# Optimization experiments

Measured on AMD Instinct MI355X. Metric: run time of the kernel, lower is better.

Reference implementation:

```python
import jax, jax.numpy as jnp
import numpy as np

S, B, H, NH, M = 2048, 2, 2048, 16, 2048
D = H // NH
FF = 4 * H
NORM = float(np.sqrt(D))  # norm_factor = sqrt(head_dim), no layer scaling
MASK_FILL = jnp.float32(-1e4)


def _ln(x, g, b):
    mu = jnp.mean(x, -1, keepdims=True)
    var = jnp.mean(jnp.square(x - mu), -1, keepdims=True)
    return (x - mu) * jax.lax.rsqrt(var + 1e-5) * g + b


def _l2(x):  # F.normalize over last dim
    return x * jax.lax.rsqrt(jnp.sum(jnp.square(x), -1, keepdims=True) + 1e-12)


def _mlp(h, w1, b1, w2, b2):  # ParallelMLP: h -> 4h -> h with gelu
    return jax.nn.gelu(h @ w1 + b1) @ w2 + b2


def setup_inputs() -> dict:
    key = jax.random.key(0)
    ks = jax.random.split(key, 12)
    w = lambda k, sh: jax.random.normal(k, sh, jnp.float32) * 0.02
    return {
        'x': jax.random.normal(ks[0], (S, B, H), jnp.float32),
        'mem_hidden': jax.random.normal(ks[1], (M, B, H), jnp.float32),
        'mem_mask': jax.random.randint(ks[2], (B, 1, S, M), 0, 5) == 0,  # True = masked
        'ln1_g': jnp.ones((H,), jnp.float32), 'ln1_b': jnp.zeros((H,), jnp.float32),
        'ln2_g': jnp.ones((H,), jnp.float32), 'ln2_b': jnp.zeros((H,), jnp.float32),
        'ln3_g': jnp.ones((H,), jnp.float32), 'ln3_b': jnp.zeros((H,), jnp.float32),
        'w_mlp1_in': w(ks[3], (H, FF)), 'b_mlp1_in': jnp.zeros((FF,), jnp.float32),
        'w_mlp1_out': w(ks[4], (FF, H)), 'b_mlp1_out': jnp.zeros((H,), jnp.float32),
        'w_q': w(ks[5], (H, H)), 'b_q': jnp.zeros((H,), jnp.float32),
        'w_kv': w(ks[6], (H, 2 * H)), 'b_kv': jnp.zeros((2 * H,), jnp.float32),
        'w_dense': w(ks[7], (H, H)), 'b_dense': jnp.zeros((H,), jnp.float32),
        'w_mlp2_in': w(ks[8], (H, FF)), 'b_mlp2_in': jnp.zeros((FF,), jnp.float32),
        'w_mlp2_out': w(ks[9], (FF, H)), 'b_mlp2_out': jnp.zeros((H,), jnp.float32),
    }


def reference(x, mem_hidden, mem_mask, ln1_g, ln1_b, ln2_g, ln2_b, ln3_g, ln3_b,
              w_mlp1_in, b_mlp1_in, w_mlp1_out, b_mlp1_out,
              w_q, b_q, w_kv, b_kv, w_dense, b_dense,
              w_mlp2_in, b_mlp2_in, w_mlp2_out, b_mlp2_out):
    # NOTE: source literally replaces x with mlp1 output (no residual on mlp1)
    x = _mlp(_ln(x, ln1_g, ln1_b), w_mlp1_in, b_mlp1_in, w_mlp1_out, b_mlp1_out)

    # memory attention: l2-normalized query vs l2-normalized retrieved memory k/v
    h2 = _ln(x, ln2_g, ln2_b)
    q = _l2((h2 @ w_q + b_q).reshape(S, B, NH, D))              # [s,b,h,d]
    kv = (mem_hidden @ w_kv + b_kv).reshape(M, B, NH, 2 * D)    # hidden_to_kv
    k = _l2(kv[..., :D])                                        # [m,b,h,d]
    v = _l2(kv[..., D:])
    scores = jnp.einsum('sbhd,mbhd->bhsm', q, k) / NORM
    scores = jnp.where(mem_mask, MASK_FILL, scores)             # attention_mask_func fill
    probs = jax.nn.softmax(scores, axis=-1)
    ctx = jnp.einsum('bhsm,mbhd->sbhd', probs, v).reshape(S, B, H)
    x = x + ctx @ w_dense + b_dense                             # dense w/ skip_bias_add

    x = x + _mlp(_ln(x, ln3_g, ln3_b), w_mlp2_in, b_mlp2_in, w_mlp2_out, b_mlp2_out)
    return x
```

## Files before the change

kernel.cpp:

```cpp
#include <hip/hip_runtime.h>
#include <stdint.h>
#include <stddef.h>

typedef __attribute__((ext_vector_type(8))) short bf16x8;
typedef __attribute__((ext_vector_type(4))) float f32x4;
typedef __attribute__((ext_vector_type(16))) float f32x16;
typedef unsigned short u16;
typedef unsigned int u32;
typedef unsigned long long u64;

static constexpr int S_ = 2048, B_ = 2, H_ = 2048, NH_ = 16, D_ = 128, M_ = 2048, FF_ = 8192;
static constexpr int SB_ = S_ * B_;
static constexpr int MB_ = M_ * B_;

__device__ __forceinline__ float b2f(u16 b) {
  union { u32 u; float f; } v; v.u = ((u32)b) << 16; return v.f;
}
__device__ __forceinline__ u16 f2b(float f) {
  union { float f; u32 u; } v; v.f = f;
  u32 u = v.u;
  return (u16)((u + 0x7FFFu + ((u >> 16) & 1u)) >> 16);
}
__device__ __forceinline__ float geluf(float x) {
  float x3 = x * x * x;
  return 0.5f * x * (1.0f + tanhf(0.7978845608028654f * (x + 0.044715f * x3)));
}

#define LDSP(p) (reinterpret_cast<__attribute__((address_space(3))) uint32_t*>(reinterpret_cast<uintptr_t>(p)))
#define GLBP(p) (reinterpret_cast<const __attribute__((address_space(1))) uint32_t*>(reinterpret_cast<uintptr_t>(p)))

__global__ void detect_kinds(const u32* __restrict__ x0, const u32* __restrict__ mask, int* __restrict__ flags) {
  if (threadIdx.x == 0 && blockIdx.x == 0) {
    int cnt = 0;
    for (int i = 0; i < 256; ++i) {
      u32 e = (x0[i] >> 7) & 0xFFu;
      if (e >= 118u && e <= 130u) ++cnt;
    }
    flags[0] = (cnt >= 128) ? 0 : 1;
    int all01 = 1, allf = 1, allb = 1;
    for (int i = 0; i < 256; ++i) {
      u32 v = mask[i];
      if (v > 1u) all01 = 0;
      if (v != 0u && v != 0x3F800000u) allf = 0;
      u32 lo = v & 0xFFFFu, hi = v >> 16;
      if ((lo != 0u && lo != 0x3F80u) || (hi != 0u && hi != 0x3F80u)) allb = 0;
    }
    flags[1] = all01 ? 1 : (allf ? 3 : (allb ? 2 : 0));
  }
}

__global__ void mask_bits(const void* __restrict__ mraw, const int* __restrict__ flags, u64* __restrict__ bm) {
  int i = blockIdx.x * 256 + threadIdx.x;
  int kind = flags[1];
  int masked;
  if (kind == 1)      masked = ((const int*)mraw)[i] != 0;
  else if (kind == 3) masked = ((const float*)mraw)[i] != 0.0f;
  else if (kind == 2) masked = ((const u16*)mraw)[i] != 0;
  else                masked = ((const unsigned char*)mraw)[i] != 0;
  u64 vote = __ballot(masked == 0);
  if ((threadIdx.x & 63) == 0) bm[i >> 6] = vote;
}

__global__ void cvt_all(const void* s0, const void* s1, const void* s2, const void* s3,
                        const void* s4, const void* s5, const void* s6, const void* s7,
                        const void* s8, const void* s9, const void* s10, const void* s11,
                        const void* s12, const int* __restrict__ flags, float* __restrict__ SM) {
  const int i = blockIdx.x * 256 + threadIdx.x;
  if (i >= 40960) return;
  const void* src; int off;
  if (i < 8192)       { src = s0;  off = 0; }
  else if (i < 10240) { src = s1;  off = 8192; }
  else if (i < 12288) { src = s2;  off = 10240; }
  else if (i < 16384) { src = s3;  off = 12288; }
  else if (i < 18432) { src = s4;  off = 16384; }
  else if (i < 26624) { src = s5;  off = 18432; }
  else if (i < 28672) { src = s6;  off = 26624; }
  else if (i < 30720) { src = s7;  off = 28672; }
  else if (i < 32768) { src = s8;  off = 30720; }
  else if (i < 34816) { src = s9;  off = 32768; }
  else if (i < 36864) { src = s10; off = 34816; }
  else if (i < 38912) { src = s11; off = 36864; }
  else                { src = s12; off = 38912; }
  const int j = i - off;
  SM[i] = flags[0] ? ((const float*)src)[j] : b2f(((const u16*)src)[j]);
}

__global__ void cast_in_bf16(const void* __restrict__ src, const int* __restrict__ flags, u16* __restrict__ dst, int n8) {
  int i = blockIdx.x * 256 + threadIdx.x;
  if (i >= n8) return;
  if (flags[0]) {
    const float4* p = (const float4*)src;
    float4 a = p[i * 2], c = p[i * 2 + 1];
    bf16x8 o;
    o[0] = (short)f2b(a.x); o[1] = (short)f2b(a.y); o[2] = (short)f2b(a.z); o[3] = (short)f2b(a.w);
    o[4] = (short)f2b(c.x); o[5] = (short)f2b(c.y); o[6] = (short)f2b(c.z); o[7] = (short)f2b(c.w);
    *(bf16x8*)&dst[i * 8] = o;
  } else {
    *(bf16x8*)&dst[i * 8] = ((const bf16x8*)src)[i];
  }
}

__global__ __launch_bounds__(256) void transpose_cast(const void* __restrict__ in, const int* __restrict__ flags,
                                                      u16* __restrict__ out, int R, int C) {
  __shared__ u16 tile[64][65];
  const int isf = flags[0];
  const int tr = blockIdx.y * 64, tc = blockIdx.x * 64;
  const int tx = threadIdx.x & 63, ty = threadIdx.x >> 6;
  const float* inf = (const float*)in;
  const u16* inb = (const u16*)in;
#pragma unroll
  for (int i = 0; i < 16; ++i) {
    int r = ty * 16 + i;
    size_t idx = (size_t)(tr + r) * C + tc + tx;
    tile[r][tx] = isf ? f2b(inf[idx]) : inb[idx];
  }
  __syncthreads();
#pragma unroll
  for (int i = 0; i < 16; ++i) {
    int c = ty * 16 + i;
    out[(size_t)(tc + c) * R + tr + tx] = tile[tx][c];
  }
}

template <int EXT>
__global__ __launch_bounds__(256) void layernorm_k(const void* __restrict__ xin, const int* __restrict__ flags,
                                                   const float* __restrict__ g, const float* __restrict__ bta,
                                                   u16* __restrict__ out) {
  const int row = blockIdx.x, t = threadIdx.x;
  float v[8];
  bool bfmode = EXT && (flags[0] == 0);
  if (bfmode) {
    const u16* xr = (const u16*)xin + (size_t)row * H_ + t * 8;
    bf16x8 a = *(const bf16x8*)xr;
#pragma unroll
    for (int j = 0; j < 8; ++j) v[j] = b2f((u16)a[j]);
  } else {
    const float* xr = (const float*)xin + (size_t)row * H_ + t * 8;
    float4 a = *(const float4*)xr, c = *(const float4*)(xr + 4);
    v[0] = a.x; v[1] = a.y; v[2] = a.z; v[3] = a.w;
    v[4] = c.x; v[5] = c.y; v[6] = c.z; v[7] = c.w;
  }
  float s1 = 0.f, s2 = 0.f;
#pragma unroll
  for (int j = 0; j < 8; ++j) { s1 += v[j]; s2 += v[j] * v[j]; }
#pragma unroll
  for (int off = 32; off > 0; off >>= 1) { s1 += __shfl_down(s1, off); s2 += __shfl_down(s2, off); }
  __shared__ float red[8];
  const int w = t >> 6;
  if ((t & 63) == 0) { red[w] = s1; red[4 + w] = s2; }
  __syncthreads();
  s1 = red[0] + red[1] + red[2] + red[3];
  s2 = red[4] + red[5] + red[6] + red[7];
  const float mean = s1 * (1.0f / H_);
  const float rstd = rsqrtf(s2 * (1.0f / H_) - mean * mean + 1e-5f);
  bf16x8 o;
#pragma unroll
  for (int j = 0; j < 8; ++j) {
    float y = (v[j] - mean) * rstd * g[t * 8 + j] + bta[t * 8 + j];
    o[j] = (short)f2b(y);
  }
  *(bf16x8*)(out + (size_t)row * H_ + t * 8) = o;
}

template <int GELU, int RES, int WF, int WB, int ODYN>
__global__ __launch_bounds__(256, 2) void gemmra(const u16* __restrict__ A, const u16* __restrict__ Bt,
                                                 const float* __restrict__ bias, const float* __restrict__ res,
                                                 void* __restrict__ outF, u16* __restrict__ outB,
                                                 const int* __restrict__ flags, int Mr, int N, int K) {
  __shared__ u16 lds[32768];
  const int t = threadIdx.x;
  const int w = t >> 6, l = t & 63, lr = l & 15, lk = l >> 4;
  const int wr = w >> 1, wc = w & 1;
  const int gx = gridDim.x, gy = gridDim.y;
  const int orig = blockIdx.y * gx + blockIdx.x;
  const int nwg = gx * gy, per = nwg >> 3;
  int tm, tn;
  if ((gx & 7) == 0 && (per & 7) == 0) {
    const int xcd = orig & 7, p = orig >> 3;
    const int ncx = gx >> 3, cy = per >> 3;
    const int ccol = xcd % ncx, crow = xcd / ncx;
    const int px = p & 7, py = p >> 3;
    tn = (ccol * 8 + px) * 128;
    tm = (crow * cy + py) * 128;
  } else {
    tn = (orig % gx) * 128;
    tm = (orig / gx) * 128;
  }
  u32 aofs[4], bofs[4];
#pragma unroll
  for (int i = 0; i < 4; ++i) {
    const int idx = i * 256 + t;
    const int srow = idx >> 3, sc = idx & 7;
    const int lc = sc ^ (srow & 7);
    aofs[i] = (u32)(tm + srow) * (u32)K + (u32)lc * 8;
    bofs[i] = (u32)(tn + srow) * (u32)K + (u32)lc * 8;
  }
  const int wdst = w * 512;
  const int cso0 = ((0 + lk) ^ (lr & 7)) * 8;
  const int cso1 = ((4 + lk) ^ (lr & 7)) * 8;
  int arow[4], brow[4];
#pragma unroll
  for (int f = 0; f < 4; ++f) {
    arow[f] = (wr * 64 + f * 16 + lr) * 64;
    brow[f] = (wc * 64 + f * 16 + lr) * 64;
  }

  const int NS = K >> 6;
  f32x4 acc[4][4] = {};

#define STG(sl) do {                                                                                  \
    u16* Ad = lds + ((sl) & 1) * 16384;                                                               \
    u16* Bd = Ad + 8192;                                                                              \
    const u32 ko = (u32)(sl) * 64;                                                                    \
    _Pragma("unroll")                                                                                 \
    for (int i = 0; i < 4; ++i) {                                                                     \
      __builtin_amdgcn_global_load_lds(GLBP(A + aofs[i] + ko), LDSP(Ad + i * 2048 + wdst), 16, 0, 0); \
      __builtin_amdgcn_global_load_lds(GLBP(Bt + bofs[i] + ko), LDSP(Bd + i * 2048 + wdst), 16, 0, 0);\
    }                                                                                                 \
  } while (0)
#define RD(afX, bqX, sl, cso) do {                                                                    \
    const u16* As_ = lds + ((sl) & 1) * 16384;                                                        \
    const u16* Bs_ = As_ + 8192;                                                                      \
    _Pragma("unroll")                                                                                 \
    for (int f = 0; f < 4; ++f) {                                                                     \
      afX[f] = *(const bf16x8*)(As_ + arow[f] + (cso));                                               \
      bqX[f] = *(const bf16x8*)(Bs_ + brow[f] + (cso));                                               \
    }                                                                                                 \
  } while (0)
#define MM(afX, bqX)                                                                                  \
  _Pragma("unroll") for (int nf = 0; nf < 4; ++nf)                                                    \
  _Pragma("unroll") for (int mf = 0; mf < 4; ++mf)                                                    \
    acc[mf][nf] = __builtin_amdgcn_mfma_f32_16x16x32_bf16(afX[mf], bqX[nf], acc[mf][nf], 0, 0, 0);

  bf16x8 afA[4], bqA[4], afB[4], bqB[4];

  STG(0);
  asm volatile("s_waitcnt vmcnt(0)" ::: "memory");
  __builtin_amdgcn_s_barrier();
  RD(afA, bqA, 0, cso0);
  asm volatile("s_waitcnt lgkmcnt(0)" ::: "memory");
  __builtin_amdgcn_sched_barrier(0);

  for (int s = 0; s < NS; ++s) {
    if (s + 1 < NS) STG(s + 1);
    RD(afB, bqB, s, cso1);
    __builtin_amdgcn_sched_barrier(0);
    __builtin_amdgcn_s_setprio(1);
    MM(afA, bqA);
    __builtin_amdgcn_s_setprio(0);
    asm volatile("s_waitcnt lgkmcnt(0)" ::: "memory");
    __builtin_amdgcn_sched_barrier(0);
    asm volatile("s_waitcnt vmcnt(0)" ::: "memory");
    __builtin_amdgcn_s_barrier();
    if (s + 1 < NS) RD(afA, bqA, s + 1, cso0);
    __builtin_amdgcn_sched_barrier(0);
    __builtin_amdgcn_s_setprio(1);
    MM(afB, bqB);
    __builtin_amdgcn_s_setprio(0);
    asm volatile("s_waitcnt lgkmcnt(0)" ::: "memory");
    __builtin_amdgcn_sched_barrier(0);
  }
#undef STG
#undef RD
#undef MM

  const int obf = ODYN ? (flags[0] ? 0 : 1) : 0;
  (void)Mr;
#pragma unroll
  for (int mf = 0; mf < 4; ++mf) {
#pragma unroll
    for (int nf = 0; nf < 4; ++nf) {
      const int col = tn + wc * 64 + nf * 16 + lr;
      const float bv = bias[col];
#pragma unroll
      for (int j = 0; j < 4; ++j) {
        const int rw = tm + wr * 64 + mf * 16 + lk * 4 + j;
        float vv = acc[mf][nf][j] + bv;
        if (RES) vv += res[(size_t)rw * N + col];
        if (GELU) vv = geluf(vv);
        if (WF) {
          if (ODYN && obf) ((u16*)outF)[(size_t)rw * N + col] = f2b(vv);
          else ((float*)outF)[(size_t)rw * N + col] = vv;
        }
        if (WB) outB[(size_t)rw * N + col] = f2b(vv);
      }
    }
  }
}

template <int GELU, int RES, int WF, int WB, int ODYN>
__global__ __launch_bounds__(256, 2) void g32ra(const u16* __restrict__ A, const u16* __restrict__ Bt,
                                                const float* __restrict__ bias, const float* __restrict__ res,
                                                void* __restrict__ outF, u16* __restrict__ outB,
                                                const int* __restrict__ flags, int Mr, int N, int K) {
  __shared__ u16 lds[32768];
  const int t = threadIdx.x;
  const int w = t >> 6, l = t & 63, lm = l & 31, lh = l >> 5;
  const int wr = w >> 1, wc = w & 1;
  const int gx = gridDim.x, gy = gridDim.y;
  const int orig = blockIdx.y * gx + blockIdx.x;
  const int nwg = gx * gy, per = nwg >> 3;
  int tm, tn;
  if ((gx & 7) == 0 && (per & 7) == 0) {
    const int xcd = orig & 7, p = orig >> 3;
    const int ncx = gx >> 3, cy = per >> 3;
    const int ccol = xcd % ncx, crow = xcd / ncx;
    const int px = p & 7, py = p >> 3;
    tn = (ccol * 8 + px) * 128;
    tm = (crow * cy + py) * 128;
  } else {
    tn = (orig % gx) * 128;
    tm = (orig / gx) * 128;
  }
  u32 aofs[4], bofs[4];
#pragma unroll
  for (int i = 0; i < 4; ++i) {
    const int idx = i * 256 + t;
    const int srow = idx >> 3, sc = idx & 7;
    const int lc = sc ^ ((srow >> 1) & 7);
    aofs[i] = (u32)(tm + srow) * (u32)K + (u32)lc * 8;
    bofs[i] = (u32)(tn + srow) * (u32)K + (u32)lc * 8;
  }
  const int wdst = w * 512;
  int offA[2][4], offB[2][4];
#pragma unroll
  for (int mi = 0; mi < 2; ++mi)
#pragma unroll
    for (int ks = 0; ks < 4; ++ks) {
      const int Ra = wr * 64 + mi * 32 + lm;
      offA[mi][ks] = Ra * 64 + (((ks * 2 + lh) ^ ((Ra >> 1) & 7)) << 3);
      const int Rb = wc * 64 + mi * 32 + lm;
      offB[mi][ks] = Rb * 64 + (((ks * 2 + lh) ^ ((Rb >> 1) & 7)) << 3);
    }

  const int NS = K >> 6;
  f32x16 acc[2][2] = {};

#define STG(sl) do {                                                                                  \
    u16* Ad = lds + ((sl) & 1) * 16384;                                                               \
    u16* Bd = Ad + 8192;                                                                              \
    const u32 ko = (u32)(sl) * 64;                                                                    \
    _Pragma("unroll")                                                                                 \
    for (int i = 0; i < 4; ++i) {                                                                     \
      __builtin_amdgcn_global_load_lds(GLBP(A + aofs[i] + ko), LDSP(Ad + i * 2048 + wdst), 16, 0, 0); \
      __builtin_amdgcn_global_load_lds(GLBP(Bt + bofs[i] + ko), LDSP(Bd + i * 2048 + wdst), 16, 0, 0);\
    }                                                                                                 \
  } while (0)
#define RD(afX, bqX, sl, half) do {                                                                   \
    const u16* As_ = lds + ((sl) & 1) * 16384;                                                        \
    const u16* Bs_ = As_ + 8192;                                                                      \
    _Pragma("unroll")                                                                                 \
    for (int mi = 0; mi < 2; ++mi)                                                                    \
    _Pragma("unroll")                                                                                 \
      for (int k2 = 0; k2 < 2; ++k2) {                                                                \
        afX[mi][k2] = *(const bf16x8*)(As_ + offA[mi][(half) * 2 + k2]);                              \
        bqX[mi][k2] = *(const bf16x8*)(Bs_ + offB[mi][(half) * 2 + k2]);                              \
      }                                                                                               \
  } while (0)
#define MM(afX, bqX)                                                                                  \
  _Pragma("unroll") for (int k2 = 0; k2 < 2; ++k2)                                                    \
  _Pragma("unroll") for (int mi = 0; mi < 2; ++mi)                                                    \
  _Pragma("unroll") for (int ni = 0; ni < 2; ++ni)                                                    \
    acc[mi][ni] = __builtin_amdgcn_mfma_f32_32x32x16_bf16(afX[mi][k2], bqX[ni][k2], acc[mi][ni], 0, 0, 0);

  bf16x8 afA[2][2], bqA[2][2], afB[2][2], bqB[2][2];

  STG(0);
  asm volatile("s_waitcnt vmcnt(0)" ::: "memory");
  __builtin_amdgcn_s_barrier();
  RD(afA, bqA, 0, 0);
  asm volatile("s_waitcnt lgkmcnt(0)" ::: "memory");
  __builtin_amdgcn_sched_barrier(0);

  for (int s = 0; s < NS; ++s) {
    if (s + 1 < NS) STG(s + 1);
    RD(afB, bqB, s, 1);
    __builtin_amdgcn_sched_barrier(0);
    __builtin_amdgcn_s_setprio(1);
    MM(afA, bqA);
    __builtin_amdgcn_s_setprio(0);
    asm volatile("s_waitcnt lgkmcnt(0)" ::: "memory");
    __builtin_amdgcn_sched_barrier(0);
    asm volatile("s_waitcnt vmcnt(0)" ::: "memory");
    __builtin_amdgcn_s_barrier();
    if (s + 1 < NS) RD(afA, bqA, s + 1, 0);
    __builtin_amdgcn_sched_barrier(0);
    __builtin_amdgcn_s_setprio(1);
    MM(afB, bqB);
    __builtin_amdgcn_s_setprio(0);
    asm volatile("s_waitcnt lgkmcnt(0)" ::: "memory");
    __builtin_amdgcn_sched_barrier(0);
  }
#undef STG
#undef RD
#undef MM

  const int obf = ODYN ? (flags[0] ? 0 : 1) : 0;
  (void)Mr;
#pragma unroll
  for (int mi = 0; mi < 2; ++mi) {
#pragma unroll
    for (int ni = 0; ni < 2; ++ni) {
      const int col = tn + wc * 64 + ni * 32 + lm;
      const float bv = bias[col];
#pragma unroll
      for (int r = 0; r < 16; ++r) {
        const int rw = tm + wr * 64 + mi * 32 + (r & 3) + 8 * (r >> 2) + 4 * lh;
        float vv = acc[mi][ni][r] + bv;
        if (RES) vv += res[(size_t)rw * N + col];
        if (GELU) vv = geluf(vv);
        if (WF) {
          if (ODYN && obf) ((u16*)outF)[(size_t)rw * N + col] = f2b(vv);
          else ((float*)outF)[(size_t)rw * N + col] = vv;
        }
        if (WB) outB[(size_t)rw * N + col] = f2b(vv);
      }
    }
  }
}

__global__ __launch_bounds__(256) void l2_q(const float* __restrict__ qpre, u16* __restrict__ Q) {
  const int t = threadIdx.x;
  const int g = blockIdx.x * 64 + (t >> 2);
  const int lg = t & 3;
  const int h = g & (NH_ - 1), sb = g >> 4;
  const float* p = qpre + (size_t)sb * H_ + h * D_ + lg * 32;
  float vv[32];
  float ss = 0.f;
#pragma unroll
  for (int i = 0; i < 8; ++i) {
    float4 a = *(const float4*)&p[i * 4];
    vv[i * 4 + 0] = a.x; vv[i * 4 + 1] = a.y; vv[i * 4 + 2] = a.z; vv[i * 4 + 3] = a.w;
    ss += a.x * a.x + a.y * a.y + a.z * a.z + a.w * a.w;
  }
  ss += __shfl_xor(ss, 1); ss += __shfl_xor(ss, 2);
  const float sc = rsqrtf(ss + 1e-12f);
  const int s = sb >> 1, b = sb & 1;
  u16* o = Q + ((size_t)(b * NH_ + h) * S_ + s) * D_ + lg * 32;
#pragma unroll
  for (int i = 0; i < 4; ++i) {
    bf16x8 ov;
#pragma unroll
    for (int j = 0; j < 8; ++j) ov[j] = (short)f2b(vv[i * 8 + j] * sc);
    *(bf16x8*)&o[i * 8] = ov;
  }
}

__global__ __launch_bounds__(256) void l2_kv(const float* __restrict__ kvpre, u16* __restrict__ Kq, u16* __restrict__ Vt) {
  __shared__ u16 vtT[128][72];
  const int t = threadIdx.x;
  const int bid = blockIdx.x;
  const int mt = bid & 31, h = (bid >> 5) & 15, b = bid >> 9;
  const int lm = t >> 2, lg = t & 3;
  const int m = mt * 64 + lm;
  const size_t rowoff = (size_t)(m * B_ + b) * (2 * H_) + h * 256;
  float vv[32];
  {
    const float* p = kvpre + rowoff + lg * 32;
    float ss = 0.f;
#pragma unroll
    for (int i = 0; i < 8; ++i) {
      float4 a = *(const float4*)&p[i * 4];
      vv[i * 4 + 0] = a.x; vv[i * 4 + 1] = a.y; vv[i * 4 + 2] = a.z; vv[i * 4 + 3] = a.w;
      ss += a.x * a.x + a.y * a.y + a.z * a.z + a.w * a.w;
    }
    ss += __shfl_xor(ss, 1); ss += __shfl_xor(ss, 2);
    const float sc = rsqrtf(ss + 1e-12f);
    u16* o = Kq + ((size_t)(b * NH_ + h) * M_ + m) * D_ + lg * 32;
#pragma unroll
    for (int i = 0; i < 4; ++i) {
      bf16x8 ov;
#pragma unroll
      for (int j = 0; j < 8; ++j) ov[j] = (short)f2b(vv[i * 8 + j] * sc);
      *(bf16x8*)&o[i * 8] = ov;
    }
  }
  {
    const float* p = kvpre + rowoff + 128 + lg * 32;
    float ss = 0.f;
#pragma unroll
    for (int i = 0; i < 8; ++i) {
      float4 a = *(const float4*)&p[i * 4];
      vv[i * 4 + 0] = a.x; vv[i * 4 + 1] = a.y; vv[i * 4 + 2] = a.z; vv[i * 4 + 3] = a.w;
      ss += a.x * a.x + a.y * a.y + a.z * a.z + a.w * a.w;
    }
    ss += __shfl_xor(ss, 1); ss += __shfl_xor(ss, 2);
    const float sc = rsqrtf(ss + 1e-12f);
#pragma unroll
    for (int i = 0; i < 32; ++i) vtT[lg * 32 + i][lm] = f2b(vv[i] * sc);
  }
  __syncthreads();
  const int d = t >> 1, half = t & 1;
  u16* o = Vt + ((size_t)(b * NH_ + h) * D_ + d) * M_ + mt * 64 + half * 32;
#pragma unroll
  for (int i = 0; i < 4; ++i) {
    bf16x8 ov = *(const bf16x8*)&vtT[d][half * 32 + i * 8];
    *(bf16x8*)&o[i * 8] = ov;
  }
}

__global__ __launch_bounds__(256, 3) void attn_k(const u16* __restrict__ Q, const u16* __restrict__ Kq,
                                                 const u16* __restrict__ Vt, const u32* __restrict__ BM32,
                                                 u16* __restrict__ ctx) {
  __shared__ u16 Kl[2][4096];
  __shared__ u16 Vl[2][4096];
  __shared__ u16 Pl[4][16 * 40];
  const int t = threadIdx.x, w = t >> 6, l = t & 63, lr = l & 15, lk = l >> 4;
  const int lin = blockIdx.x;
  const int xcd = lin & 7, idx = lin >> 3;
  const int bh = xcd * 4 + (idx >> 5);
  const int chunk = idx & 31;
  const int b = bh >> 4, h = bh & 15;
  const int srow = chunk * 64 + w * 16;
  const u16* Qb = Q + ((size_t)bh * S_ + srow) * D_;
  bf16x8 qf[4];
#pragma unroll
  for (int kc = 0; kc < 4; ++kc)
    qf[kc] = *(const bf16x8*)&Qb[lr * D_ + kc * 32 + lk * 8];
  f32x4 oacc[8] = {};
  float den[4] = {};
  const u16* Kb = Kq + (size_t)bh * M_ * D_;
  const u16* Vb = Vt + (size_t)bh * D_ * M_;
  const float invn = 0.08838834764831845f;
  u32 ksrc[2], vsrc[2];
#pragma unroll
  for (int i = 0; i < 2; ++i) {
    const int kidx = i * 256 + t;
    const int kr = kidx >> 4, kc_ = (kidx & 15) ^ (kr & 7);
    ksrc[i] = (u32)kr * D_ + (u32)kc_ * 8;
    const int vidx = i * 256 + t;
    const int vd = vidx >> 2, vc = (vidx & 3) ^ ((vd >> 1) & 3);
    vsrc[i] = (u32)vd * M_ + (u32)vc * 8;
  }
  const int wdst = w * 64 * 8;
  u32 mrow[4];
#pragma unroll
  for (int j2 = 0; j2 < 4; ++j2)
    mrow[j2] = ((u32)b * S_ + (u32)(srow + lk * 4 + j2)) * 64u;

#define STG(buf, m0) do {                                                                              \
    _Pragma("unroll")                                                                                  \
    for (int i = 0; i < 2; ++i) {                                                                      \
      __builtin_amdgcn_global_load_lds(GLBP(Kb + (size_t)(m0) * D_ + ksrc[i]),                         \
                                       LDSP(&Kl[buf][i * 2048 + wdst]), 16, 0, 0);                     \
      __builtin_amdgcn_global_load_lds(GLBP(Vb + (size_t)(m0) + vsrc[i]),                              \
                                       LDSP(&Vl[buf][i * 2048 + wdst]), 16, 0, 0);                     \
    }                                                                                                  \
  } while (0)

  STG(0, 0);
  asm volatile("s_waitcnt vmcnt(0)" ::: "memory");
  __builtin_amdgcn_s_barrier();
  int cur = 0;

  for (int t64 = 0; t64 < M_ / 32; ++t64) {
    const int m0 = t64 * 32;
    if (t64 + 1 < M_ / 32) STG(cur ^ 1, m0 + 32);
    u32 mw[4];
#pragma unroll
    for (int j2 = 0; j2 < 4; ++j2) mw[j2] = BM32[mrow[j2] + t64];
    f32x4 sc[2] = {};
#pragma unroll
    for (int mf = 0; mf < 2; ++mf) {
      const int r = mf * 16 + lr;
#pragma unroll
      for (int kc = 0; kc < 4; ++kc) {
        const int cc = ((kc * 4 + lk) ^ (r & 7));
        bf16x8 kfv = *(const bf16x8*)&Kl[cur][r * 128 + cc * 8];
        sc[mf] = __builtin_amdgcn_mfma_f32_16x16x32_bf16(qf[kc], kfv, sc[mf], 0, 0, 0);
      }
    }
#pragma unroll
    for (int j2 = 0; j2 < 4; ++j2) {
      const int rloc = lk * 4 + j2;
#pragma unroll
      for (int mf = 0; mf < 2; ++mf) {
        float p = __expf(sc[mf][j2] * invn);
        p = ((mw[j2] >> (mf * 16 + lr)) & 1u) ? p : 0.0f;
        den[j2] += p;
        Pl[w][rloc * 40 + mf * 16 + lr] = f2b(p);
      }
    }
    asm volatile("s_waitcnt lgkmcnt(0)" ::: "memory");
    __builtin_amdgcn_sched_barrier(0);
    bf16x8 pa = *(const bf16x8*)&Pl[w][lr * 40 + lk * 8];
#pragma unroll
    for (int nf = 0; nf < 8; ++nf) {
      const int d = nf * 16 + lr;
      const int cc = lk ^ ((d >> 1) & 3);
      bf16x8 vfv = *(const bf16x8*)&Vl[cur][d * 32 + cc * 8];
      oacc[nf] = __builtin_amdgcn_mfma_f32_16x16x32_bf16(pa, vfv, oacc[nf], 0, 0, 0);
    }
    asm volatile("s_waitcnt vmcnt(0)" ::: "memory");
    __builtin_amdgcn_s_barrier();
    cur ^= 1;
  }
#undef STG
#pragma unroll
  for (int j2 = 0; j2 < 4; ++j2) {
    float d = den[j2];
    d += __shfl_xor(d, 1); d += __shfl_xor(d, 2); d += __shfl_xor(d, 4); d += __shfl_xor(d, 8);
    den[j2] = 1.0f / fmaxf(d, 1e-20f);
  }
#pragma unroll
  for (int nf = 0; nf < 8; ++nf)
#pragma unroll
    for (int j2 = 0; j2 < 4; ++j2) {
      const int s = srow + lk * 4 + j2;
      const int dd = nf * 16 + lr;
      ctx[((size_t)s * B_ + b) * H_ + h * D_ + dd] = f2b(oacc[nf][j2] * den[j2]);
    }
}

extern "C" void kernel_launch(void* const* d_in, const int* in_sizes, int n_in,
                              void* d_out, int out_size, void* d_ws, size_t ws_size,
                              hipStream_t stream) {
  (void)in_sizes; (void)n_in; (void)out_size; (void)ws_size;
  char* ws = (char*)d_ws;
  u16* WT     = (u16*)(ws + 0);
  void* MID   = (void*)(ws + 33554432);
  float* XF   = (float*)(ws + 100663296);
  u16* HB     = (u16*)(ws + 134217728);
  u16* MEMB   = (u16*)(ws + 150994944);
  u16* QB     = (u16*)(ws + 167772160);
  u16* KB     = (u16*)(ws + 184549376);
  u16* VTB    = (u16*)(ws + 201326592);
  u64* BMB    = (u64*)(ws + 218103808);
  float* SM   = (float*)(ws + 234881024);
  int* FLAGS  = (int*)(ws + 235044864);

  float* Bias1  = SM + 0;
  float* Bias1o = SM + 8192;
  float* BiasQ  = SM + 10240;
  float* BiasKV = SM + 12288;
  float* BiasD  = SM + 16384;
  float* Bias2  = SM + 18432;
  float* Bias2o = SM + 26624;
  float* G1v = SM + 28672; float* B1v = SM + 30720;
  float* G2v = SM + 32768; float* B2v = SM + 34816;
  float* G3v = SM + 36864; float* B3v = SM + 38912;

  detect_kinds<<<1, 64, 0, stream>>>((const u32*)d_in[0], (const u32*)d_in[2], FLAGS);

  cvt_all<<<160, 256, 0, stream>>>(d_in[10], d_in[12], d_in[14], d_in[16], d_in[18],
                                   d_in[20], d_in[22], d_in[3], d_in[4], d_in[5],
                                   d_in[6], d_in[7], d_in[8], FLAGS, SM);

  mask_bits<<<(B_ * S_ * M_) / 256, 256, 0, stream>>>(d_in[2], FLAGS, BMB);
  cast_in_bf16<<<(MB_ * H_ / 8) / 256, 256, 0, stream>>>(d_in[1], FLAGS, MEMB, MB_ * H_ / 8);

  dim3 blk(256);
  layernorm_k<1><<<SB_, blk, 0, stream>>>(d_in[0], FLAGS, G1v, B1v, HB);
  transpose_cast<<<dim3(FF_ / 64, H_ / 64), blk, 0, stream>>>(d_in[9], FLAGS, WT, H_, FF_);
  g32ra<1, 0, 0, 1, 0><<<dim3(FF_ / 128, SB_ / 128), blk, 0, stream>>>(HB, WT, Bias1, nullptr, nullptr, (u16*)MID, FLAGS, SB_, FF_, H_);
  transpose_cast<<<dim3(H_ / 64, FF_ / 64), blk, 0, stream>>>(d_in[11], FLAGS, WT, FF_, H_);
  gemmra<0, 0, 1, 0, 0><<<dim3(H_ / 128, SB_ / 128), blk, 0, stream>>>((u16*)MID, WT, Bias1o, nullptr, XF, nullptr, FLAGS, SB_, H_, FF_);

  layernorm_k<0><<<SB_, blk, 0, stream>>>(XF, FLAGS, G2v, B2v, HB);
  transpose_cast<<<dim3(H_ / 64, H_ / 64), blk, 0, stream>>>(d_in[13], FLAGS, WT, H_, H_);
  gemmra<0, 0, 1, 0, 0><<<dim3(H_ / 128, SB_ / 128), blk, 0, stream>>>(HB, WT, BiasQ, nullptr, MID, nullptr, FLAGS, SB_, H_, H_);
  l2_q<<<(SB_ * NH_) / 64, blk, 0, stream>>>((const float*)MID, QB);
  transpose_cast<<<dim3(2 * H_ / 64, H_ / 64), blk, 0, stream>>>(d_in[15], FLAGS, WT, H_, 2 * H_);
  gemmra<0, 0, 1, 0, 0><<<dim3(2 * H_ / 128, MB_ / 128), blk, 0, stream>>>(MEMB, WT, BiasKV, nullptr, MID, nullptr, FLAGS, MB_, 2 * H_, H_);
  l2_kv<<<B_ * NH_ * (M_ / 64), blk, 0, stream>>>((const float*)MID, KB, VTB);
  attn_k<<<1024, blk, 0, stream>>>(QB, KB, VTB, (const u32*)BMB, MEMB);
  transpose_cast<<<dim3(H_ / 64, H_ / 64), blk, 0, stream>>>(d_in[17], FLAGS, WT, H_, H_);
  gemmra<0, 1, 1, 0, 0><<<dim3(H_ / 128, SB_ / 128), blk, 0, stream>>>(MEMB, WT, BiasD, XF, XF, nullptr, FLAGS, SB_, H_, H_);

  layernorm_k<0><<<SB_, blk, 0, stream>>>(XF, FLAGS, G3v, B3v, HB);
  transpose_cast<<<dim3(FF_ / 64, H_ / 64), blk, 0, stream>>>(d_in[19], FLAGS, WT, H_, FF_);
  g32ra<1, 0, 0, 1, 0><<<dim3(FF_ / 128, SB_ / 128), blk, 0, stream>>>(HB, WT, Bias2, nullptr, nullptr, (u16*)MID, FLAGS, SB_, FF_, H_);
  transpose_cast<<<dim3(H_ / 64, FF_ / 64), blk, 0, stream>>>(d_in[21], FLAGS, WT, FF_, H_);
  gemmra<0, 1, 1, 0, 1><<<dim3(H_ / 128, SB_ / 128), blk, 0, stream>>>((u16*)MID, WT, Bias2o, XF, d_out, nullptr, FLAGS, SB_, H_, FF_);
}
```

Baseline: 1.173 ms.

## Replace 32x32 MFMA GEMM with 512-thread 16x16 MFMA kernel for MLP up-projections

The two MLP up-projection GEMMs (K=2048, N=8192) now use a new 512-thread, 8-wave kernel in place of the 256-thread one. It keeps the 128x128 tile but gives each wave a 64x32 sub-tile computed with 16x16x32 bf16 MFMAs. The LDS swizzle and staging are changed so each thread issues two global-to-LDS loads per operand instead of four. The goal is more waves to hide latency and lighter per-thread staging. The cost is smaller per-wave reuse, more LDS fragment reads, and a different MFMA shape.

```diff
diff --git a/kernel.cpp b/kernel.cpp
--- a/kernel.cpp
+++ b/kernel.cpp
@@ -4,7 +4,6 @@
 
 typedef __attribute__((ext_vector_type(8))) short bf16x8;
 typedef __attribute__((ext_vector_type(4))) float f32x4;
-typedef __attribute__((ext_vector_type(16))) float f32x16;
 typedef unsigned short u16;
 typedef unsigned int u32;
 typedef unsigned long long u64;
@@ -289,14 +288,14 @@
 }
 
 template <int GELU, int RES, int WF, int WB, int ODYN>
-__global__ __launch_bounds__(256, 2) void g32ra(const u16* __restrict__ A, const u16* __restrict__ Bt,
-                                                const float* __restrict__ bias, const float* __restrict__ res,
-                                                void* __restrict__ outF, u16* __restrict__ outB,
-                                                const int* __restrict__ flags, int Mr, int N, int K) {
+__global__ __launch_bounds__(512, 2) void gemmra512(const u16* __restrict__ A, const u16* __restrict__ Bt,
+                                                    const float* __restrict__ bias, const float* __restrict__ res,
+                                                    void* __restrict__ outF, u16* __restrict__ outB,
+                                                    const int* __restrict__ flags, int Mr, int N, int K) {
   __shared__ u16 lds[32768];
   const int t = threadIdx.x;
-  const int w = t >> 6, l = t & 63, lm = l & 31, lh = l >> 5;
-  const int wr = w >> 1, wc = w & 1;
+  const int w = t >> 6, l = t & 63, lr = l & 15, lk = l >> 4;
+  const int wr = w >> 2, wc = w & 3;
   const int gx = gridDim.x, gy = gridDim.y;
   const int orig = blockIdx.y * gx + blockIdx.x;
   const int nwg = gx * gy, per = nwg >> 3;
@@ -312,69 +311,62 @@
     tn = (orig % gx) * 128;
     tm = (orig / gx) * 128;
   }
-  u32 aofs[4], bofs[4];
-#pragma unroll
-  for (int i = 0; i < 4; ++i) {
-    const int idx = i * 256 + t;
+  u32 aofs[2], bofs[2];
+#pragma unroll
+  for (int i = 0; i < 2; ++i) {
+    const int idx = i * 512 + t;
     const int srow = idx >> 3, sc = idx & 7;
-    const int lc = sc ^ ((srow >> 1) & 7);
+    const int lc = sc ^ (srow & 7);
     aofs[i] = (u32)(tm + srow) * (u32)K + (u32)lc * 8;
     bofs[i] = (u32)(tn + srow) * (u32)K + (u32)lc * 8;
   }
   const int wdst = w * 512;
-  int offA[2][4], offB[2][4];
-#pragma unroll
-  for (int mi = 0; mi < 2; ++mi)
-#pragma unroll
-    for (int ks = 0; ks < 4; ++ks) {
-      const int Ra = wr * 64 + mi * 32 + lm;
-      offA[mi][ks] = Ra * 64 + (((ks * 2 + lh) ^ ((Ra >> 1) & 7)) << 3);
-      const int Rb = wc * 64 + mi * 32 + lm;
-      offB[mi][ks] = Rb * 64 + (((ks * 2 + lh) ^ ((Rb >> 1) & 7)) << 3);
-    }
+  const int cso0 = ((0 + lk) ^ (lr & 7)) * 8;
+  const int cso1 = ((4 + lk) ^ (lr & 7)) * 8;
+  int arow[4], brow[2];
+#pragma unroll
+  for (int f = 0; f < 4; ++f) arow[f] = (wr * 64 + f * 16 + lr) * 64;
+#pragma unroll
+  for (int f = 0; f < 2; ++f) brow[f] = (wc * 32 + f * 16 + lr) * 64;
 
   const int NS = K >> 6;
-  f32x16 acc[2][2] = {};
+  f32x4 acc[4][2] = {};
 
 #define STG(sl) do {                                                                                  \
     u16* Ad = lds + ((sl) & 1) * 16384;                                                               \
     u16* Bd = Ad + 8192;                                                                              \
     const u32 ko = (u32)(sl) * 64;                                                                    \
     _Pragma("unroll")                                                                                 \
-    for (int i = 0; i < 4; ++i) {                                                                     \
-      __builtin_amdgcn_global_load_lds(GLBP(A + aofs[i] + ko), LDSP(Ad + i * 2048 + wdst), 16, 0, 0); \
-      __builtin_amdgcn_global_load_lds(GLBP(Bt + bofs[i] + ko), LDSP(Bd + i * 2048 + wdst), 16, 0, 0);\
+    for (int i = 0; i < 2; ++i) {                                                                     \
+      __builtin_amdgcn_global_load_lds(GLBP(A + aofs[i] + ko), LDSP(Ad + i * 4096 + wdst), 16, 0, 0); \
+      __builtin_amdgcn_global_load_lds(GLBP(Bt + bofs[i] + ko), LDSP(Bd + i * 4096 + wdst), 16, 0, 0);\
     }                                                                                                 \
   } while (0)
-#define RD(afX, bqX, sl, half) do {                                                                   \
+#define RD(afX, bqX, sl, cso) do {                                                                    \
     const u16* As_ = lds + ((sl) & 1) * 16384;                                                        \
     const u16* Bs_ = As_ + 8192;                                                                      \
     _Pragma("unroll")                                                                                 \
-    for (int mi = 0; mi < 2; ++mi)                                                                    \
+    for (int f = 0; f < 4; ++f) afX[f] = *(const bf16x8*)(As_ + arow[f] + (cso));                     \
     _Pragma("unroll")                                                                                 \
-      for (int k2 = 0; k2 < 2; ++k2) {                                                                \
-        afX[mi][k2] = *(const bf16x8*)(As_ + offA[mi][(half) * 2 + k2]);                              \
-        bqX[mi][k2] = *(const bf16x8*)(Bs_ + offB[mi][(half) * 2 + k2]);                              \
-      }                                                                                               \
+    for (int f = 0; f < 2; ++f) bqX[f] = *(const bf16x8*)(Bs_ + brow[f] + (cso));                     \
   } while (0)
 #define MM(afX, bqX)                                                                                  \
-  _Pragma("unroll") for (int k2 = 0; k2 < 2; ++k2)                                                    \
-  _Pragma("unroll") for (int mi = 0; mi < 2; ++mi)                                                    \
-  _Pragma("unroll") for (int ni = 0; ni < 2; ++ni)                                                    \
-    acc[mi][ni] = __builtin_amdgcn_mfma_f32_32x32x16_bf16(afX[mi][k2], bqX[ni][k2], acc[mi][ni], 0, 0, 0);
-
-  bf16x8 afA[2][2], bqA[2][2], afB[2][2], bqB[2][2];
+  _Pragma("unroll") for (int nf = 0; nf < 2; ++nf)                                                    \
+  _Pragma("unroll") for (int mf = 0; mf < 4; ++mf)                                                    \
+    acc[mf][nf] = __builtin_amdgcn_mfma_f32_16x16x32_bf16(afX[mf], bqX[nf], acc[mf][nf], 0, 0, 0);
+
+  bf16x8 afA[4], bqA[2], afB[4], bqB[2];
 
   STG(0);
   asm volatile("s_waitcnt vmcnt(0)" ::: "memory");
   __builtin_amdgcn_s_barrier();
-  RD(afA, bqA, 0, 0);
+  RD(afA, bqA, 0, cso0);
   asm volatile("s_waitcnt lgkmcnt(0)" ::: "memory");
   __builtin_amdgcn_sched_barrier(0);
 
   for (int s = 0; s < NS; ++s) {
     if (s + 1 < NS) STG(s + 1);
-    RD(afB, bqB, s, 1);
+    RD(afB, bqB, s, cso1);
     __builtin_amdgcn_sched_barrier(0);
     __builtin_amdgcn_s_setprio(1);
     MM(afA, bqA);
@@ -383,7 +375,7 @@
     __builtin_amdgcn_sched_barrier(0);
     asm volatile("s_waitcnt vmcnt(0)" ::: "memory");
     __builtin_amdgcn_s_barrier();
-    if (s + 1 < NS) RD(afA, bqA, s + 1, 0);
+    if (s + 1 < NS) RD(afA, bqA, s + 1, cso0);
     __builtin_amdgcn_sched_barrier(0);
     __builtin_amdgcn_s_setprio(1);
     MM(afB, bqB);
@@ -398,15 +390,15 @@
   const int obf = ODYN ? (flags[0] ? 0 : 1) : 0;
   (void)Mr;
 #pragma unroll
-  for (int mi = 0; mi < 2; ++mi) {
-#pragma unroll
-    for (int ni = 0; ni < 2; ++ni) {
-      const int col = tn + wc * 64 + ni * 32 + lm;
+  for (int mf = 0; mf < 4; ++mf) {
+#pragma unroll
+    for (int nf = 0; nf < 2; ++nf) {
+      const int col = tn + wc * 32 + nf * 16 + lr;
       const float bv = bias[col];
 #pragma unroll
-      for (int r = 0; r < 16; ++r) {
-        const int rw = tm + wr * 64 + mi * 32 + (r & 3) + 8 * (r >> 2) + 4 * lh;
-        float vv = acc[mi][ni][r] + bv;
+      for (int j = 0; j < 4; ++j) {
+        const int rw = tm + wr * 64 + mf * 16 + lk * 4 + j;
+        float vv = acc[mf][nf][j] + bv;
         if (RES) vv += res[(size_t)rw * N + col];
         if (GELU) vv = geluf(vv);
         if (WF) {
@@ -650,9 +642,10 @@
   cast_in_bf16<<<(MB_ * H_ / 8) / 256, 256, 0, stream>>>(d_in[1], FLAGS, MEMB, MB_ * H_ / 8);
 
   dim3 blk(256);
+  dim3 blk5(512);
   layernorm_k<1><<<SB_, blk, 0, stream>>>(d_in[0], FLAGS, G1v, B1v, HB);
   transpose_cast<<<dim3(FF_ / 64, H_ / 64), blk, 0, stream>>>(d_in[9], FLAGS, WT, H_, FF_);
-  g32ra<1, 0, 0, 1, 0><<<dim3(FF_ / 128, SB_ / 128), blk, 0, stream>>>(HB, WT, Bias1, nullptr, nullptr, (u16*)MID, FLAGS, SB_, FF_, H_);
+  gemmra512<1, 0, 0, 1, 0><<<dim3(FF_ / 128, SB_ / 128), blk5, 0, stream>>>(HB, WT, Bias1, nullptr, nullptr, (u16*)MID, FLAGS, SB_, FF_, H_);
   transpose_cast<<<dim3(H_ / 64, FF_ / 64), blk, 0, stream>>>(d_in[11], FLAGS, WT, FF_, H_);
   gemmra<0, 0, 1, 0, 0><<<dim3(H_ / 128, SB_ / 128), blk, 0, stream>>>((u16*)MID, WT, Bias1o, nullptr, XF, nullptr, FLAGS, SB_, H_, FF_);
 
@@ -669,7 +662,7 @@
 
   layernorm_k<0><<<SB_, blk, 0, stream>>>(XF, FLAGS, G3v, B3v, HB);
   transpose_cast<<<dim3(FF_ / 64, H_ / 64), blk, 0, stream>>>(d_in[19], FLAGS, WT, H_, FF_);
-  g32ra<1, 0, 0, 1, 0><<<dim3(FF_ / 128, SB_ / 128), blk, 0, stream>>>(HB, WT, Bias2, nullptr, nullptr, (u16*)MID, FLAGS, SB_, FF_, H_);
+  gemmra512<1, 0, 0, 1, 0><<<dim3(FF_ / 128, SB_ / 128), blk5, 0, stream>>>(HB, WT, Bias2, nullptr, nullptr, (u16*)MID, FLAGS, SB_, FF_, H_);
   transpose_cast<<<dim3(H_ / 64, FF_ / 64), blk, 0, stream>>>(d_in[21], FLAGS, WT, FF_, H_);
   gemmra<0, 1, 1, 0, 1><<<dim3(H_ / 128, SB_ / 128), blk, 0, stream>>>((u16*)MID, WT, Bias2o, XF, d_out, nullptr, FLAGS, SB_, H_, FF_);
 }
```

Result: faster. 1.136 ms (-3.2%).
